# Kernel optimization log

Measured on AMD Instinct MI355X. Metric: run time of the kernel, lower is better.

## Reference

```python
import jax, jax.numpy as jnp
import numpy as np
from jax import lax

B, T, CD = 128, 4096, 2
HID, K = 64, 5
FIN = CD * 3 + 4  # 10 scorer input channels
PAD = K // 2
LEARNED_W = 0.5


def setup_inputs() -> dict:
    key = jax.random.key(0)
    ks = jax.random.split(key, 10)
    trajectory = jax.random.normal(ks[0], (B, T, CD), jnp.float32)
    intervals = jax.random.uniform(ks[1], (B, T), jnp.float32, 0.01, 1.0)
    lengths = jax.random.randint(ks[2], (B,), T // 2, T + 1)
    attention_mask = (jnp.arange(T)[None, :] < lengths[:, None]).astype(jnp.float32)
    observed_mask = (jax.random.uniform(ks[3], (B, T)) > 0.3).astype(jnp.float32)
    w1 = jax.random.normal(ks[4], (HID, FIN, K), jnp.float32) / np.sqrt(FIN * K)
    b1 = jnp.zeros((HID,), jnp.float32)
    w2 = jax.random.normal(ks[5], (HID, HID, K), jnp.float32) / np.sqrt(HID * K)
    b2 = jnp.zeros((HID,), jnp.float32)
    w3 = jax.random.normal(ks[6], (1, HID, 1), jnp.float32) / np.sqrt(HID)
    b3 = jnp.zeros((1,), jnp.float32)
    return dict(trajectory=trajectory, intervals=intervals, attention_mask=attention_mask,
                observed_mask=observed_mask, w1=w1, b1=b1, w2=w2, b2=b2, w3=w3, b3=b3)


def _conv1d(x, w, pad):  # x: [B,C,T], w: [O,I,K]
    return lax.conv_general_dilated(x, w, (1,), [(pad, pad)],
                                    dimension_numbers=('NCH', 'OIH', 'NCH'))


def _safe_norm(v):  # grad-safe L2 norm over last dim, exact forward
    s2 = jnp.sum(v * v, axis=-1)
    return jnp.where(s2 > 0, jnp.sqrt(jnp.where(s2 > 0, s2, 1.0)), 0.0)


def _robust_normalize(values, mask):
    # vectorized version of per-sample 95th-percentile scaling
    valid = mask > 0.5
    n = jnp.sum(valid, axis=1)  # [B] int
    s = jnp.sort(jnp.where(valid, values, jnp.inf), axis=1)  # valid ascending, inf last
    idx = jnp.maximum(1, jnp.ceil(n.astype(jnp.float32) * 0.95).astype(jnp.int32)) - 1
    idx = jnp.clip(idx, 0, T - 1)
    scale = jnp.abs(jnp.take_along_axis(s, idx[:, None], axis=1))[:, 0]
    maxabs = jnp.max(jnp.where(valid, jnp.abs(values), 0.0), axis=1)
    scale = jnp.where(scale < 1e-6, maxabs, scale)
    out = values / jnp.maximum(scale, 1e-6)[:, None]
    out = jnp.where((n > 0)[:, None], out, 0.0)
    return out * mask


def _smooth(scores, mask):  # avg_pool1d k=K stride 1 pad K//2 (count_include_pad=True)
    kern = jnp.full((1, 1, K), 1.0 / K, scores.dtype)
    sm = _conv1d(scores[:, None, :], kern, PAD)[:, 0]
    return sm * mask


def _forward(trajectory, intervals, attention_mask, observed_mask, w1, b1, w2, b2, w3, b3):
    mask = attention_mask
    vm = mask > 0.5
    pm = (vm[:, 1:] & vm[:, :-1]).astype(trajectory.dtype)  # [B,T-1]

    def mdiff3(x):
        d = (x[:, 1:] - x[:, :-1]) * pm[..., None]
        return jnp.concatenate([jnp.zeros_like(x[:, :1]), d], axis=1)

    def mdiff2(x):
        d = (x[:, 1:] - x[:, :-1]) * pm
        return jnp.concatenate([jnp.zeros_like(x[:, :1]), d], axis=1)

    mt = trajectory * mask[..., None]
    coord_diff = mdiff3(mt)
    delta_t = jnp.maximum(intervals[..., None], 1e-3)
    interval_feat = intervals * mask
    velocity = coord_diff / delta_t * mask[..., None]
    acceleration = mdiff3(velocity) / delta_t * mask[..., None]
    speed = _safe_norm(velocity) * mask
    speed_change = jnp.abs(mdiff2(speed)) * mask
    accel_norm = _safe_norm(acceleration) * mask
    heading = jnp.arctan2(velocity[..., 1], velocity[..., 0])
    rhc = heading[:, 1:] - heading[:, :-1]
    rhc = jnp.abs(jnp.arctan2(jnp.sin(rhc), jnp.cos(rhc)))
    heading_change = jnp.concatenate([jnp.zeros_like(speed[:, :1]), rhc * pm], axis=1) * mask
    obs_feat = observed_mask * mask
    ot = jnp.abs(observed_mask[:, 1:] - observed_mask[:, :-1]) * pm
    observed_transition = jnp.concatenate([jnp.zeros_like(speed[:, :1]), ot], axis=1) * mask

    feats = jnp.concatenate([mt, velocity, acceleration, speed[..., None],
                             heading_change[..., None], interval_feat[..., None],
                             obs_feat[..., None]], axis=-1) * mask[..., None]  # [B,T,10]

    # rule scores
    scores = (0.35 * _robust_normalize(heading_change, mask)
              + 0.30 * _robust_normalize(accel_norm, mask)
              + 0.25 * _robust_normalize(speed_change, mask)
              + 0.10 * jnp.clip(observed_transition, 0.0, 1.0) * mask)
    scores = _smooth(scores, mask)
    rule_scores = jnp.clip(_robust_normalize(scores, mask), 0.0, 1.0) * mask

    # learned scores (Conv1d stack, exact GELU like torch default)
    x = feats.transpose(0, 2, 1)  # [B,10,T]
    h = jax.nn.gelu(_conv1d(x, w1, PAD) + b1[None, :, None], approximate=False)
    h = jax.nn.gelu(_conv1d(h, w2, PAD) + b2[None, :, None], approximate=False)
    learned = jax.nn.sigmoid((_conv1d(h, w3, 0) + b3[None, :, None])[:, 0]) * mask
    learned = jnp.clip(_smooth(learned, mask), 0.0, 1.0)

    out = (1.0 - LEARNED_W) * rule_scores + LEARNED_W * learned
    return jnp.clip(out, 0.0, 1.0) * mask


def reference(trajectory, intervals, attention_mask, observed_mask, w1, b1, w2, b2, w3, b3):
    return _forward(trajectory, intervals, attention_mask, observed_mask, w1, b1, w2, b2, w3, b3)
```

## Files before the change

### kernel.cpp

```cpp
#include <hip/hip_runtime.h>

namespace {

constexpr int B_ = 128;
constexpr int T_ = 4096;
constexpr int BT = B_ * T_;
constexpr int TTILE = 128;
constexpr unsigned NOINS = 0xFFFFFFFFu;

constexpr size_t OFF_W1F   = 0;
constexpr size_t OFF_W2F   = 2048;
constexpr size_t OFF_FEATS = 16384;
constexpr size_t OFF_RULE  = OFF_FEATS + (size_t)B_ * 10 * T_;
constexpr size_t OFF_LP    = OFF_RULE + (size_t)BT;

typedef _Float16 half8 __attribute__((ext_vector_type(8)));
typedef _Float16 half4 __attribute__((ext_vector_type(4)));
typedef _Float16 half2_t __attribute__((ext_vector_type(2)));
typedef float f32x4 __attribute__((ext_vector_type(4)));

__device__ __forceinline__ float clip01(float x) { return fminf(fmaxf(x, 0.f), 1.f); }

__device__ __forceinline__ float gelu_fast(float x) {
  float s = x * 0.7071067811865475f;
  float a = fabsf(s);
  float t = __builtin_amdgcn_rcpf(__builtin_fmaf(0.3275911f, a, 1.0f));
  float p = __builtin_fmaf(t, 1.061405429f, -1.453152027f);
  p = __builtin_fmaf(t, p, 1.421413741f);
  p = __builtin_fmaf(t, p, -0.284496736f);
  p = __builtin_fmaf(t, p, 0.254829592f);
  p = p * t;
  float e = __builtin_amdgcn_exp2f(a * a * -1.4426950408889634f);
  float erfa = __builtin_fmaf(-p, e, 1.0f);
  float erfs = copysignf(erfa, s);
  return 0.5f * x * (1.0f + erfs);
}

__device__ __forceinline__ void compute_feats(
    const float* __restrict__ tr, const float* __restrict__ iv,
    const float* __restrict__ mk, const float* __restrict__ om, int t,
    float* __restrict__ f , float* anv_out, float* scv_out, float* otv_out) {
  float m  = mk[t];
  float m1 = (t >= 1) ? mk[t - 1] : 0.f;
  float m2 = (t >= 2) ? mk[t - 2] : 0.f;
  float pm01 = (m > 0.5f && m1 > 0.5f) ? 1.f : 0.f;
  float pm12 = (m1 > 0.5f && m2 > 0.5f) ? 1.f : 0.f;
  float x0x = tr[2 * t] * m, x0y = tr[2 * t + 1] * m;
  float x1x = 0.f, x1y = 0.f, x2x = 0.f, x2y = 0.f;
  if (t >= 1) { x1x = tr[2 * (t - 1)] * m1; x1y = tr[2 * (t - 1) + 1] * m1; }
  if (t >= 2) { x2x = tr[2 * (t - 2)] * m2; x2y = tr[2 * (t - 2) + 1] * m2; }
  float dt0 = fmaxf(iv[t], 1e-3f);
  float dt1 = (t >= 1) ? fmaxf(iv[t - 1], 1e-3f) : 1e-3f;
  float vx = 0.f, vy = 0.f, v1x = 0.f, v1y = 0.f;
  if (t >= 1) { vx = (x0x - x1x) * pm01 / dt0 * m; vy = (x0y - x1y) * pm01 / dt0 * m; }
  if (t >= 2) { v1x = (x1x - x2x) * pm12 / dt1 * m1; v1y = (x1y - x2y) * pm12 / dt1 * m1; }
  float ax = 0.f, ay = 0.f;
  if (t >= 1) { ax = (vx - v1x) * pm01 / dt0 * m; ay = (vy - v1y) * pm01 / dt0 * m; }
  float s2 = vx * vx + vy * vy;
  float speed = (s2 > 0.f ? sqrtf(s2) : 0.f) * m;
  float s21 = v1x * v1x + v1y * v1y;
  float speed1 = (s21 > 0.f ? sqrtf(s21) : 0.f) * m1;
  float scv = (t >= 1) ? fabsf((speed - speed1) * pm01) * m : 0.f;
  float a2 = ax * ax + ay * ay;
  float anv = (a2 > 0.f ? sqrtf(a2) : 0.f) * m;
  float hcv = 0.f;
  if (t >= 1) {
    bool z0 = (vx == 0.f && vy == 0.f);
    bool z1 = (v1x == 0.f && v1y == 0.f);
    float yy, xx;
    if (z1)      { yy = vy;  xx = vx; }
    else if (z0) { yy = v1y; xx = v1x; }
    else { yy = vy * v1x - vx * v1y; xx = vx * v1x + vy * v1y; }
    hcv = fabsf(atan2f(yy, xx)) * pm01 * m;
  }
  float obs = om[t] * m;
  float otv = (t >= 1) ? fminf(fabsf(om[t] - om[t - 1]) * pm01 * m, 1.f) : 0.f;
  float itf = iv[t] * m;
  f[0] = x0x; f[1] = x0y; f[2] = vx; f[3] = vy; f[4] = ax; f[5] = ay;
  f[6] = speed; f[7] = hcv; f[8] = itf; f[9] = obs;
  *anv_out = anv; *scv_out = scv; *otv_out = otv;
}

template <int CHUNK, int NB>
__device__ __forceinline__ void find_bucket_1k(const unsigned* __restrict__ hist,
                                               unsigned* selb, unsigned* selk,
                                               unsigned* sW, int tid) {
  unsigned k = *selk;
  unsigned vals[CHUNK];
  unsigned ps = 0;
#pragma unroll
  for (int c = 0; c < CHUNK; ++c) {
    int idx = tid * CHUNK + c;
    unsigned v = (idx < NB) ? hist[idx] : 0u;
    vals[c] = v; ps += v;
  }
  unsigned incl = ps;
  int lane = tid & 63;
#pragma unroll
  for (int off = 1; off < 64; off <<= 1) {
    unsigned tv = __shfl_up(incl, off, 64);
    if (lane >= off) incl += tv;
  }
  if (lane == 63) sW[tid >> 6] = incl;
  __syncthreads();
  int wid = tid >> 6;
  unsigned woff = 0;
  for (int i = 0; i < wid; ++i) woff += sW[i];
  incl += woff;
  unsigned excl = incl - ps;
  __syncthreads();
  if (excl <= k && k < incl) {
    unsigned run = excl;
    int c = 0;
#pragma unroll
    for (; c < CHUNK - 1; ++c) {
      if (run + vals[c] > k) break;
      run += vals[c];
    }
    *selb = (unsigned)(tid * CHUNK + c);
    *selk = k - run;
  }
  __syncthreads();
}

__device__ __forceinline__ float radix_select_1k(const unsigned* u, unsigned k,
                                                 unsigned* hist, unsigned* selb,
                                                 unsigned* selk, unsigned* sW, int tid) {
  for (int i = tid; i < 4096; i += 1024) hist[i] = 0u;
  if (tid == 0) *selk = k;
  __syncthreads();
#pragma unroll
  for (int r = 0; r < 4; ++r)
    if (u[r] != NOINS) atomicAdd(&hist[u[r] >> 20], 1u);
  __syncthreads();
  find_bucket_1k<4, 4096>(hist, selb, selk, sW, tid);
  unsigned p1 = *selb;
  for (int i = tid; i < 4096; i += 1024) hist[i] = 0u;
  __syncthreads();
#pragma unroll
  for (int r = 0; r < 4; ++r)
    if (u[r] != NOINS && (u[r] >> 20) == p1) atomicAdd(&hist[(u[r] >> 8) & 0xFFFu], 1u);
  __syncthreads();
  find_bucket_1k<4, 4096>(hist, selb, selk, sW, tid);
  unsigned p2 = *selb;
  unsigned pref = (p1 << 12) | p2;
  if (tid < 256) hist[tid] = 0u;
  __syncthreads();
#pragma unroll
  for (int r = 0; r < 4; ++r)
    if (u[r] != NOINS && (u[r] >> 8) == pref) atomicAdd(&hist[u[r] & 0xFFu], 1u);
  __syncthreads();
  find_bucket_1k<1, 256>(hist, selb, selk, sW, tid);
  unsigned p3 = *selb;
  __syncthreads();
  return __uint_as_float((p1 << 20) | (p2 << 8) | p3);
}

__device__ __forceinline__ float block_max_1k(float v, float* sM, int tid) {
#pragma unroll
  for (int off = 32; off; off >>= 1) v = fmaxf(v, __shfl_xor(v, off));
  if ((tid & 63) == 0) sM[tid >> 6] = v;
  __syncthreads();
  float m = sM[0];
#pragma unroll
  for (int i = 1; i < 16; ++i) m = fmaxf(m, sM[i]);
  __syncthreads();
  return m;
}

__global__ __launch_bounds__(1024)
void rulefuse_k(const float* __restrict__ traj, const float* __restrict__ intervals,
                const float* __restrict__ amask, const float* __restrict__ omask,
                float* __restrict__ feats, float* __restrict__ rule) {
  __shared__ unsigned hist[4096];
  __shared__ unsigned sW[16];
  __shared__ unsigned selb, selk;
  __shared__ float vbuf[4096];
  __shared__ float sM[16];
  __shared__ int iCnt[16];
  __shared__ int n_sh;
  __shared__ float scale_sh[3];
  int b = blockIdx.x, tid = threadIdx.x;
  const float* tr = traj + (size_t)b * T_ * 2;
  const float* iv = intervals + (size_t)b * T_;
  const float* mk = amask + (size_t)b * T_;
  const float* om = omask + (size_t)b * T_;
  float* frow = feats + (size_t)b * 10 * T_;

  float hcv[4], anv[4], scv[4], otv[4], mreg[4];
  int cnt = 0;
  for (int r = 0; r < 4; ++r) {
    int t = tid + 1024 * r;
    float f[10], a, s, o;
    compute_feats(tr, iv, mk, om, t, f, &a, &s, &o);
#pragma unroll
    for (int c = 0; c < 10; ++c) frow[(size_t)c * T_ + t] = f[c];
    hcv[r] = f[7]; anv[r] = a; scv[r] = s; otv[r] = o;
    mreg[r] = mk[t];
    cnt += (mreg[r] > 0.5f);
  }
#pragma unroll
  for (int off = 32; off; off >>= 1) cnt += __shfl_xor(cnt, off);
  if ((tid & 63) == 0) iCnt[tid >> 6] = cnt;
  __syncthreads();
  if (tid == 0) {
    int n = 0;
#pragma unroll
    for (int i = 0; i < 16; ++i) n += iCnt[i];
    n_sh = n;
  }
  __syncthreads();
  int n = n_sh;
  int cidx = (int)ceilf((float)n * 0.95f);
  if (cidx < 1) cidx = 1;
  int kidx = cidx - 1;
  if (kidx < 0) kidx = 0;
  if (kidx > T_ - 1) kidx = T_ - 1;

  for (int m3 = 0; m3 < 3; ++m3) {
    unsigned u[4];
    float mx = 0.f;
#pragma unroll
    for (int r = 0; r < 4; ++r) {
      float v = (m3 == 0 ? hcv[r] : m3 == 1 ? anv[r] : scv[r]);
      if (mreg[r] > 0.5f) {
        mx = fmaxf(mx, fabsf(v));
        unsigned ub = __float_as_uint(v);
        if ((int)ub < 0) ub = 0u;
        u[r] = ub;
      } else u[r] = NOINS;
    }
    mx = block_max_1k(mx, sM, tid);
    float kth = fabsf(radix_select_1k(u, (unsigned)kidx, hist, &selb, &selk, sW, tid));
    if (tid == 0) {
      float s = (kth < 1e-6f) ? mx : kth;
      scale_sh[m3] = fmaxf(s, 1e-6f);
    }
  }
  __syncthreads();
  float sc0 = scale_sh[0], sc1 = scale_sh[1], sc2 = scale_sh[2];
#pragma unroll
  for (int r = 0; r < 4; ++r) {
    int t = tid + 1024 * r;
    float v = 0.f;
    if (n > 0) {
      v = 0.35f * (hcv[r] / sc0) + 0.30f * (anv[r] / sc1)
        + 0.25f * (scv[r] / sc2) + 0.10f * otv[r];
    }
    vbuf[t] = v;
  }
  __syncthreads();
  float sm[4];
#pragma unroll
  for (int r = 0; r < 4; ++r) {
    int t = tid + 1024 * r;
    float s = 0.f;
#pragma unroll
    for (int d = -2; d <= 2; ++d) {
      int tt = t + d;
      if (tt >= 0 && tt < T_) s += vbuf[tt];
    }
    sm[r] = s * 0.2f * mreg[r];
  }
  unsigned u2[4];
  float mx2 = 0.f;
#pragma unroll
  for (int r = 0; r < 4; ++r) {
    if (mreg[r] > 0.5f) {
      mx2 = fmaxf(mx2, fabsf(sm[r]));
      unsigned ub = __float_as_uint(sm[r]);
      if ((int)ub < 0) ub = 0u;
      u2[r] = ub;
    } else u2[r] = NOINS;
  }
  mx2 = block_max_1k(mx2, sM, tid);
  float kth4 = fabsf(radix_select_1k(u2, (unsigned)kidx, hist, &selb, &selk, sW, tid));
  float scale4 = fmaxf((kth4 < 1e-6f) ? mx2 : kth4, 1e-6f);
  float* rrow = rule + (size_t)b * T_;
#pragma unroll
  for (int r = 0; r < 4; ++r) {
    int t = tid + 1024 * r;
    float v = (n > 0) ? sm[r] / scale4 : 0.f;
    rrow[t] = clip01(v) * mreg[r];
  }
}

__global__ __launch_bounds__(256)
void repack_k(const float* __restrict__ w1g, const float* __restrict__ w2g,
              half8* __restrict__ w1f, half8* __restrict__ w2f) {
  int gid = blockIdx.x * 256 + threadIdx.x;
  if (gid >= 48 * 64) return;
  int fid = gid >> 6, lane = gid & 63;
  int qd = lane >> 4, ln = lane & 15;
  half8 v;
  if (fid < 8) {
    int m = fid >> 1, kk = fid & 1;
    int o = m * 16 + ln;
#pragma unroll
    for (int j = 0; j < 8; ++j) {
      int ck = kk * 32 + qd * 8 + j;
      float val = 0.f;
      if (ck < 50) { int k_ = ck / 10, c = ck - 10 * k_; val = w1g[o * 50 + c * 5 + k_]; }
      v[j] = (_Float16)val;
    }
    w1f[fid * 64 + lane] = v;
  } else {
    int f2 = fid - 8;
    int k = f2 >> 3, kk = (f2 >> 2) & 1, m = f2 & 3;
    int o = m * 16 + ln;
#pragma unroll
    for (int j = 0; j < 8; ++j) {
      int ic = kk * 32 + qd * 8 + j;
      v[j] = (_Float16)w2g[o * 320 + ic * 5 + k];
    }
    w2f[f2 * 64 + lane] = v;
  }
}

__global__ __launch_bounds__(512, 4)
void conv_k(const float* __restrict__ feats, const half8* __restrict__ w1f,
            const float* __restrict__ b1g, const half8* __restrict__ w2f,
            const float* __restrict__ b2g, const float* __restrict__ w3g,
            const float* __restrict__ b3g, const float* __restrict__ amask,
            float* __restrict__ lp) {
  __shared__ _Float16 sIm[144 * 72];
  __shared__ _Float16 sH1[132 * 72];
  __shared__ float sF[10 * 136];
  __shared__ float sPart[2][128];
  int tid = threadIdx.x;
  int lane = tid & 63, w = tid >> 6;
  int qd = lane >> 4, ln = lane & 15;
  int tile = blockIdx.x, b = blockIdx.y;
  int t0 = tile * TTILE;
  const float* frow = feats + (size_t)b * 10 * T_;

  for (int s = tid; s < 1360; s += 512) {
    int c = s / 136, u = s - c * 136;
    int t = t0 - 4 + u;
    sF[s] = (t >= 0 && t < T_) ? frow[(size_t)c * T_ + t] * 0.015625f : 0.f;
  }
  for (int s = tid; s < 144 * 7; s += 512) {
    int jt = s / 7, d = s - jt * 7;
    *reinterpret_cast<unsigned*>(&sIm[jt * 72 + 50 + 2 * d]) = 0u;
  }
  __syncthreads();
  for (int s = tid; s < 660; s += 512) {
    int jt = s / 5, k = s - jt * 5;
#pragma unroll
    for (int cp = 0; cp < 5; ++cp) {
      float lo = sF[(2 * cp) * 136 + jt + k];
      float hi = sF[(2 * cp + 1) * 136 + jt + k];
      half2_t pk;
      pk[0] = (_Float16)lo;
      pk[1] = (_Float16)hi;
      *reinterpret_cast<half2_t*>(&sIm[jt * 72 + k * 10 + 2 * cp]) = pk;
    }
  }
  __syncthreads();

  half8 a1[4][2];
#pragma unroll
  for (int m = 0; m < 4; ++m)
#pragma unroll
    for (int kk = 0; kk < 2; ++kk) a1[m][kk] = w1f[(m * 2 + kk) * 64 + lane];

  for (int n0 = w; n0 < 9; n0 += 8) {
    int jt = n0 * 16 + ln;
    half8 bf0 = *reinterpret_cast<const half8*>(&sIm[jt * 72 + qd * 8]);
    half8 bf1 = *reinterpret_cast<const half8*>(&sIm[jt * 72 + 32 + qd * 8]);
#pragma unroll
    for (int m = 0; m < 4; ++m) {
      f32x4 acc;
      f32x4 bv = *reinterpret_cast<const f32x4*>(&b1g[m * 16 + qd * 4]);
#pragma unroll
      for (int r = 0; r < 4; ++r) acc[r] = bv[r] * 0.015625f;
      acc = __builtin_amdgcn_mfma_f32_16x16x32_f16(a1[m][0], bf0, acc, 0, 0, 0);
      acc = __builtin_amdgcn_mfma_f32_16x16x32_f16(a1[m][1], bf1, acc, 0, 0, 0);
      if (jt < 132) {
        int t = t0 - 2 + jt;
        bool inr = (t >= 0 && t < T_);
        half4 hv;
#pragma unroll
        for (int r = 0; r < 4; ++r) {
          float h = inr ? gelu_fast(acc[r] * 64.f) * 0.0625f : 0.f;
          hv[r] = (_Float16)h;
        }
        *reinterpret_cast<half4*>(&sH1[jt * 72 + m * 16 + qd * 4]) = hv;
      }
    }
  }
  __syncthreads();

  int p = w & 1, nq = w >> 1;
  f32x4 acc2[2][2];
#pragma unroll
  for (int dm = 0; dm < 2; ++dm) {
    f32x4 bv = *reinterpret_cast<const f32x4*>(&b2g[(2 * p + dm) * 16 + qd * 4]);
#pragma unroll
    for (int dn = 0; dn < 2; ++dn)
#pragma unroll
      for (int r = 0; r < 4; ++r) acc2[dm][dn][r] = bv[r] * 0.0625f;
  }
#pragma unroll
  for (int k = 0; k < 5; ++k) {
#pragma unroll
    for (int kk = 0; kk < 2; ++kk) {
      half8 A0 = w2f[((k * 2 + kk) * 4 + 2 * p + 0) * 64 + lane];
      half8 A1 = w2f[((k * 2 + kk) * 4 + 2 * p + 1) * 64 + lane];
      half8 B0 = *reinterpret_cast<const half8*>(
          &sH1[((2 * nq + 0) * 16 + ln + k) * 72 + kk * 32 + qd * 8]);
      half8 B1 = *reinterpret_cast<const half8*>(
          &sH1[((2 * nq + 1) * 16 + ln + k) * 72 + kk * 32 + qd * 8]);
      acc2[0][0] = __builtin_amdgcn_mfma_f32_16x16x32_f16(A0, B0, acc2[0][0], 0, 0, 0);
      acc2[0][1] = __builtin_amdgcn_mfma_f32_16x16x32_f16(A0, B1, acc2[0][1], 0, 0, 0);
      acc2[1][0] = __builtin_amdgcn_mfma_f32_16x16x32_f16(A1, B0, acc2[1][0], 0, 0, 0);
      acc2[1][1] = __builtin_amdgcn_mfma_f32_16x16x32_f16(A1, B1, acc2[1][1], 0, 0, 0);
    }
  }
  f32x4 w3a = *reinterpret_cast<const f32x4*>(&w3g[(2 * p + 0) * 16 + qd * 4]);
  f32x4 w3b = *reinterpret_cast<const f32x4*>(&w3g[(2 * p + 1) * 16 + qd * 4]);
#pragma unroll
  for (int dn = 0; dn < 2; ++dn) {
    float s = 0.f;
#pragma unroll
    for (int r = 0; r < 4; ++r) s += w3a[r] * gelu_fast(acc2[0][dn][r] * 16.f);
#pragma unroll
    for (int r = 0; r < 4; ++r) s += w3b[r] * gelu_fast(acc2[1][dn][r] * 16.f);
    s += __shfl_xor(s, 16);
    s += __shfl_xor(s, 32);
    if (lane < 16) sPart[p][(2 * nq + dn) * 16 + lane] = s;
  }
  __syncthreads();
  if (tid < 128) {
    int t = t0 + tid;
    float logit = sPart[0][tid] + sPart[1][tid] + b3g[0];
    float m = amask[(size_t)b * T_ + t];
    lp[(size_t)b * T_ + t] = (1.f / (1.f + expf(-logit))) * m;
  }
}

__global__ __launch_bounds__(256)
void final_k(const float* __restrict__ rule, const float* __restrict__ lp,
             const float* __restrict__ amask, float* __restrict__ out) {
  int idx = blockIdx.x * 256 + threadIdx.x;
  if (idx >= BT) return;
  int t = idx & (T_ - 1);
  float s = 0.f;
#pragma unroll
  for (int d = -2; d <= 2; ++d) {
    int tt = t + d;
    if (tt >= 0 && tt < T_) s += lp[idx + d];
  }
  float m = amask[idx];
  float learned = clip01(s * 0.2f * m);
  out[idx] = clip01(0.5f * rule[idx] + 0.5f * learned) * m;
}

}

extern "C" void kernel_launch(void* const* d_in, const int* in_sizes, int n_in,
                              void* d_out, int out_size, void* d_ws, size_t ws_size,
                              hipStream_t stream) {
  const float* traj      = (const float*)d_in[0];
  const float* intervals = (const float*)d_in[1];
  const float* amask     = (const float*)d_in[2];
  const float* omask     = (const float*)d_in[3];
  const float* w1        = (const float*)d_in[4];
  const float* b1        = (const float*)d_in[5];
  const float* w2        = (const float*)d_in[6];
  const float* b2        = (const float*)d_in[7];
  const float* w3        = (const float*)d_in[8];
  const float* b3        = (const float*)d_in[9];
  float* out = (float*)d_out;
  float* ws = (float*)d_ws;

  float* feats = ws + OFF_FEATS;
  float* rule  = ws + OFF_RULE;
  float* lp    = ws + OFF_LP;
  half8* w1f = (half8*)(ws + OFF_W1F);
  half8* w2f = (half8*)(ws + OFF_W2F);

  repack_k<<<12, 256, 0, stream>>>(w1, w2, w1f, w2f);
  rulefuse_k<<<B_, 1024, 0, stream>>>(traj, intervals, amask, omask, feats, rule);
  conv_k<<<dim3(T_ / TTILE, B_), 512, 0, stream>>>(feats, w1f, b1, w2f, b2, w3, b3,
                                                   amask, lp);
  final_k<<<BT / 256, 256, 0, stream>>>(rule, lp, amask, out);
}
```

Measured before the change: 184.2 us.

## Split feature computation into a wide grid kernel and merge weight repack

Feature computation moves out of the 128-block rule kernel into a new fully parallel kernel with one thread per (b,t). That kernel writes the conv features plus four rule-score inputs to workspace, and its first blocks also repack the conv weights, so the separate repack launch goes away. The rule kernel now only loads the precomputed values and runs the percentile selection. The aim is to stop the heavy feature math from running on only 128 blocks, at the cost of about 8 MB of extra global traffic for the intermediate arrays.

```diff
diff --git a/kernel.cpp b/kernel.cpp
--- a/kernel.cpp
+++ b/kernel.cpp
@@ -11,7 +11,11 @@
 constexpr size_t OFF_W1F   = 0;
 constexpr size_t OFF_W2F   = 2048;
 constexpr size_t OFF_FEATS = 16384;
-constexpr size_t OFF_RULE  = OFF_FEATS + (size_t)B_ * 10 * T_;
+constexpr size_t OFF_HC    = OFF_FEATS + (size_t)B_ * 10 * T_;
+constexpr size_t OFF_AN    = OFF_HC + (size_t)BT;
+constexpr size_t OFF_SC    = OFF_AN + (size_t)BT;
+constexpr size_t OFF_OT    = OFF_SC + (size_t)BT;
+constexpr size_t OFF_RULE  = OFF_OT + (size_t)BT;
 constexpr size_t OFF_LP    = OFF_RULE + (size_t)BT;
 
 typedef _Float16 half8 __attribute__((ext_vector_type(8)));
@@ -81,6 +85,56 @@
   *anv_out = anv; *scv_out = scv; *otv_out = otv;
 }
 
+__global__ __launch_bounds__(256)
+void featurize_k(const float* __restrict__ traj, const float* __restrict__ intervals,
+                 const float* __restrict__ amask, const float* __restrict__ omask,
+                 const float* __restrict__ w1g, const float* __restrict__ w2g,
+                 float* __restrict__ feats, float* __restrict__ hc, float* __restrict__ an,
+                 float* __restrict__ sc, float* __restrict__ ot,
+                 half8* __restrict__ w1f, half8* __restrict__ w2f) {
+  int idx = blockIdx.x * 256 + threadIdx.x;
+  int b = idx >> 12;
+  int t = idx & (T_ - 1);
+  float f[10], anv, scv, otv;
+  compute_feats(traj + (size_t)b * T_ * 2, intervals + (size_t)b * T_,
+                amask + (size_t)b * T_, omask + (size_t)b * T_, t, f, &anv, &scv, &otv);
+  float* frow = feats + (size_t)b * 10 * T_;
+#pragma unroll
+  for (int c = 0; c < 10; ++c) frow[(size_t)c * T_ + t] = f[c];
+  hc[idx] = f[7]; an[idx] = anv; sc[idx] = scv; ot[idx] = otv;
+
+  if (blockIdx.x < 12) {
+    int gid = blockIdx.x * 256 + threadIdx.x;
+    if (gid < 48 * 64) {
+      int fid = gid >> 6, lane = gid & 63;
+      int qd = lane >> 4, ln = lane & 15;
+      half8 v;
+      if (fid < 8) {
+        int m = fid >> 1, kk = fid & 1;
+        int o = m * 16 + ln;
+#pragma unroll
+        for (int j = 0; j < 8; ++j) {
+          int ck = kk * 32 + qd * 8 + j;
+          float val = 0.f;
+          if (ck < 50) { int k_ = ck / 10, c = ck - 10 * k_; val = w1g[o * 50 + c * 5 + k_]; }
+          v[j] = (_Float16)val;
+        }
+        w1f[fid * 64 + lane] = v;
+      } else {
+        int f2 = fid - 8;
+        int k = f2 >> 3, kk = (f2 >> 2) & 1, m = f2 & 3;
+        int o = m * 16 + ln;
+#pragma unroll
+        for (int j = 0; j < 8; ++j) {
+          int ic = kk * 32 + qd * 8 + j;
+          v[j] = (_Float16)w2g[o * 320 + ic * 5 + k];
+        }
+        w2f[f2 * 64 + lane] = v;
+      }
+    }
+  }
+}
+
 template <int CHUNK, int NB>
 __device__ __forceinline__ void find_bucket_1k(const unsigned* __restrict__ hist,
                                                unsigned* selb, unsigned* selk,
@@ -169,9 +223,9 @@
 }
 
 __global__ __launch_bounds__(1024)
-void rulefuse_k(const float* __restrict__ traj, const float* __restrict__ intervals,
-                const float* __restrict__ amask, const float* __restrict__ omask,
-                float* __restrict__ feats, float* __restrict__ rule) {
+void ruleselect_k(const float* __restrict__ hc, const float* __restrict__ an,
+                  const float* __restrict__ sc, const float* __restrict__ ot,
+                  const float* __restrict__ amask, float* __restrict__ rule) {
   __shared__ unsigned hist[4096];
   __shared__ unsigned sW[16];
   __shared__ unsigned selb, selk;
@@ -181,21 +235,18 @@
   __shared__ int n_sh;
   __shared__ float scale_sh[3];
   int b = blockIdx.x, tid = threadIdx.x;
-  const float* tr = traj + (size_t)b * T_ * 2;
-  const float* iv = intervals + (size_t)b * T_;
   const float* mk = amask + (size_t)b * T_;
-  const float* om = omask + (size_t)b * T_;
-  float* frow = feats + (size_t)b * 10 * T_;
+  const float* hrow = hc + (size_t)b * T_;
+  const float* arow = an + (size_t)b * T_;
+  const float* srow = sc + (size_t)b * T_;
+  const float* orow = ot + (size_t)b * T_;
 
   float hcv[4], anv[4], scv[4], otv[4], mreg[4];
   int cnt = 0;
+#pragma unroll
   for (int r = 0; r < 4; ++r) {
     int t = tid + 1024 * r;
-    float f[10], a, s, o;
-    compute_feats(tr, iv, mk, om, t, f, &a, &s, &o);
-#pragma unroll
-    for (int c = 0; c < 10; ++c) frow[(size_t)c * T_ + t] = f[c];
-    hcv[r] = f[7]; anv[r] = a; scv[r] = s; otv[r] = o;
+    hcv[r] = hrow[t]; anv[r] = arow[t]; scv[r] = srow[t]; otv[r] = orow[t];
     mreg[r] = mk[t];
     cnt += (mreg[r] > 0.5f);
   }
@@ -282,38 +333,6 @@
     int t = tid + 1024 * r;
     float v = (n > 0) ? sm[r] / scale4 : 0.f;
     rrow[t] = clip01(v) * mreg[r];
-  }
-}
-
-__global__ __launch_bounds__(256)
-void repack_k(const float* __restrict__ w1g, const float* __restrict__ w2g,
-              half8* __restrict__ w1f, half8* __restrict__ w2f) {
-  int gid = blockIdx.x * 256 + threadIdx.x;
-  if (gid >= 48 * 64) return;
-  int fid = gid >> 6, lane = gid & 63;
-  int qd = lane >> 4, ln = lane & 15;
-  half8 v;
-  if (fid < 8) {
-    int m = fid >> 1, kk = fid & 1;
-    int o = m * 16 + ln;
-#pragma unroll
-    for (int j = 0; j < 8; ++j) {
-      int ck = kk * 32 + qd * 8 + j;
-      float val = 0.f;
-      if (ck < 50) { int k_ = ck / 10, c = ck - 10 * k_; val = w1g[o * 50 + c * 5 + k_]; }
-      v[j] = (_Float16)val;
-    }
-    w1f[fid * 64 + lane] = v;
-  } else {
-    int f2 = fid - 8;
-    int k = f2 >> 3, kk = (f2 >> 2) & 1, m = f2 & 3;
-    int o = m * 16 + ln;
-#pragma unroll
-    for (int j = 0; j < 8; ++j) {
-      int ic = kk * 32 + qd * 8 + j;
-      v[j] = (_Float16)w2g[o * 320 + ic * 5 + k];
-    }
-    w2f[f2 * 64 + lane] = v;
   }
 }
 
@@ -475,13 +494,18 @@
   float* ws = (float*)d_ws;
 
   float* feats = ws + OFF_FEATS;
+  float* hc    = ws + OFF_HC;
+  float* an    = ws + OFF_AN;
+  float* sc    = ws + OFF_SC;
+  float* ot    = ws + OFF_OT;
   float* rule  = ws + OFF_RULE;
   float* lp    = ws + OFF_LP;
   half8* w1f = (half8*)(ws + OFF_W1F);
   half8* w2f = (half8*)(ws + OFF_W2F);
 
-  repack_k<<<12, 256, 0, stream>>>(w1, w2, w1f, w2f);
-  rulefuse_k<<<B_, 1024, 0, stream>>>(traj, intervals, amask, omask, feats, rule);
+  featurize_k<<<BT / 256, 256, 0, stream>>>(traj, intervals, amask, omask, w1, w2,
+                                            feats, hc, an, sc, ot, w1f, w2f);
+  ruleselect_k<<<B_, 1024, 0, stream>>>(hc, an, sc, ot, amask, rule);
   conv_k<<<dim3(T_ / TTILE, B_), 512, 0, stream>>>(feats, w1f, b1, w2f, b2, w3, b3,
                                                    amask, lp);
   final_k<<<BT / 256, 256, 0, stream>>>(rule, lp, amask, out);
```

Result: no change. 181.7 us (-1.3%).
